# Optimization experiments

Measured on AMD Instinct MI355X. Metric: run time of the kernel, lower is better.

## Reference

```python
import jax, jax.numpy as jnp
import numpy as np
from jax import lax

N = 100000
E = 1600000
IN_C = 128
HID = 128
OUT_C = 64
NUM_CLASSES = 40
BN_EPS = 1e-5


def gcn_conv(x, row, col, W, b):
    # x: [N, F_in] -> [N, F_out]; PyG GCNConv: self-loops + sym normalization
    h = x @ W                                   # [N, F_out]
    loops = jnp.arange(N, dtype=row.dtype)
    r = jnp.concatenate([row, loops])           # [E+N]
    c = jnp.concatenate([col, loops])
    ones = jnp.ones(r.shape[0], dtype=x.dtype)
    deg = jax.ops.segment_sum(ones, c, num_segments=N)
    dinv = jnp.where(deg > 0, lax.rsqrt(deg), jnp.zeros_like(deg))
    norm = dinv[r] * dinv[c]                    # [E+N]
    msg = h[r] * norm[:, None]                  # gather + scale  [E+N, F_out]
    out = jax.ops.segment_sum(msg, c, num_segments=N)
    return out + b


def setup_inputs() -> dict:
    key = jax.random.key(0)
    ks = jax.random.split(key, 16)
    def glorot(k, shape):
        lim = float(np.sqrt(6.0 / (shape[0] + shape[1])))
        return jax.random.uniform(k, shape, jnp.float32, -lim, lim)
    x = jax.random.normal(ks[0], (N, IN_C), jnp.float32)
    edge_index = jax.random.randint(ks[1], (2, E), 0, N, jnp.int64)
    return {
        "x": x,
        "edge_index": edge_index,
        "w1": glorot(ks[2], (IN_C, HID)), "b1": jnp.zeros((HID,), jnp.float32),
        "w2": glorot(ks[3], (HID, HID)), "b2": jnp.zeros((HID,), jnp.float32),
        "bn_gamma": jnp.ones((HID,), jnp.float32), "bn_beta": jnp.zeros((HID,), jnp.float32),
        "bn_mean": jnp.zeros((HID,), jnp.float32), "bn_var": jnp.ones((HID,), jnp.float32),
        "cls_w": glorot(ks[4], (HID, OUT_C)), "cls_b": jnp.zeros((OUT_C,), jnp.float32),
        "sim_w": glorot(ks[5], (HID, NUM_CLASSES)), "sim_b": jnp.zeros((NUM_CLASSES,), jnp.float32),
        "hom_w": glorot(ks[6], (HID, 1)), "hom_b": jnp.zeros((1,), jnp.float32),
        "ent_w": glorot(ks[7], (HID, 1)), "ent_b": jnp.zeros((1,), jnp.float32),
    }


def reference(x, edge_index, w1, b1, w2, b2, bn_gamma, bn_beta, bn_mean, bn_var,
              cls_w, cls_b, sim_w, sim_b, hom_w, hom_b, ent_w, ent_b):
    row, col = edge_index[0], edge_index[1]
    # layer 1: GCNConv -> BN (eval) -> ReLU (dropout is identity in eval)
    h = gcn_conv(x, row, col, w1, b1)
    h = (h - bn_mean) * lax.rsqrt(bn_var + BN_EPS) * bn_gamma + bn_beta
    h = jax.nn.relu(h)
    # layer 2
    h = gcn_conv(h, row, col, w2, b2)
    main_out = jax.nn.log_softmax(h @ cls_w + cls_b, axis=1)
    sim_out = jax.nn.softmax(h @ sim_w + sim_b, axis=1)
    hom_out = jax.nn.sigmoid((h @ hom_w + hom_b)[:, 0])
    ent_out = jax.nn.sigmoid((h @ ent_w + ent_b)[:, 0])
    return (main_out, sim_out, hom_out, ent_out)
```

## Files before the change

### kernel.cpp

```cpp
#include <hip/hip_runtime.h>
#include <hip/hip_bf16.h>
#include <math.h>

#define N_NODES 100000
#define N_EDGES 1600000
#define F 128
#define OUT_C 64
#define NUM_CLASSES 40
#define BN_EPS 1e-5f

#define NBUCK 782
#define BCAP 4096
#define FILL_BLOCKS 512
#define EPB ((N_EDGES + FILL_BLOCKS - 1) / FILL_BLOCKS)
#define FILL_ITERS 13

#define PSC 0
#define POF 128
#define PFB2 256

typedef __hip_bfloat16 bf16;
typedef __attribute__((ext_vector_type(8))) short bf16x8;
typedef __attribute__((ext_vector_type(4))) float f32x4;

struct ParamSegs {
    const void* src[16];
    int dst[16];
};

__device__ __forceinline__ float uasf(unsigned u) { return __uint_as_float(u); }
__device__ __forceinline__ unsigned f2bu(float f) {
    bf16 h = __float2bfloat16(f);
    return (unsigned)*(unsigned short*)&h;
}
__device__ __forceinline__ float ldp(const void* p, int i, int isf) {
    return isf ? ((const float*)p)[i] : __bfloat162float(((const bf16*)p)[i]);
}
__device__ __forceinline__ int load_edge(const int* __restrict__ ei, int which, int i, int i64) {
    size_t elem = (size_t)which * N_EDGES + (size_t)i;
    return i64 ? ei[elem * 2] : ei[elem];
}
__device__ __forceinline__ int detect_isf(const void* x, int t, int* sflag) {
    if (t < 64) {
        unsigned w = ((const unsigned*)x)[t];
        unsigned e = (w >> 23) & 0xFFu;
        unsigned long long m = __ballot(w == 0u || (e >= 90u && e <= 160u));
        if (t == 0) *sflag = (__popcll(m) >= 48) ? 1 : 0;
    }
    __syncthreads();
    return *sflag;
}
__device__ __forceinline__ int detect_i64(const void* ei, int t, int* sflag) {
    if (t < 64) {
        unsigned long long m = __ballot(((const unsigned*)ei)[2 * t + 1] == 0u);
        if (t == 0) *sflag = (__popcll(m) >= 60) ? 1 : 0;
    }
    __syncthreads();
    return *sflag;
}
__device__ __forceinline__ void head_src(const ParamSegs& segs, int c, const void** hp, int* hb,
                                         int* hs) {
    if (c < OUT_C) {
        *hp = segs.src[8];
        *hb = c;
        *hs = OUT_C;
    } else if (c < OUT_C + NUM_CLASSES) {
        *hp = segs.src[10];
        *hb = c - OUT_C;
        *hs = NUM_CLASSES;
    } else if (c == 104) {
        *hp = segs.src[12];
        *hb = 0;
        *hs = 1;
    } else if (c == 105) {
        *hp = segs.src[14];
        *hb = 0;
        *hs = 1;
    } else {
        *hp = nullptr;
        *hb = 0;
        *hs = 0;
    }
}

#define ACC8(u)                                \
    do {                                       \
        a[0] += uasf((u).x << 16);             \
        a[1] += uasf((u).x & 0xFFFF0000u);     \
        a[2] += uasf((u).y << 16);             \
        a[3] += uasf((u).y & 0xFFFF0000u);     \
        a[4] += uasf((u).z << 16);             \
        a[5] += uasf((u).z & 0xFFFF0000u);     \
        a[6] += uasf((u).w << 16);             \
        a[7] += uasf((u).w & 0xFFFF0000u);     \
    } while (0)

__global__ __launch_bounds__(256) void fill2_kernel(const int* __restrict__ ei,
                                                    int* __restrict__ bcur,
                                                    int* __restrict__ srcBuck) {
    __shared__ int hist[NBUCK];
    __shared__ int gbase[NBUCK];
    __shared__ int lcur[NBUCK];
    __shared__ int sflag;
    int blk = blockIdx.x;
    int t = threadIdx.x;
    int i64 = detect_i64(ei, t, &sflag);
    int e0 = blk * EPB;
    int ecnt = N_EDGES - e0;
    if (ecnt > EPB) ecnt = EPB;
    for (int i = t; i < NBUCK; i += 256) hist[i] = 0;
    __syncthreads();
    int ccache[FILL_ITERS];
#pragma unroll
    for (int it = 0; it < FILL_ITERS; ++it) {
        int i = t + it * 256;
        int c = -1;
        if (i < ecnt) {
            c = load_edge(ei, 1, e0 + i, i64);
            atomicAdd(&hist[c >> 7], 1);
        }
        ccache[it] = c;
    }
    __syncthreads();
    for (int i = t; i < NBUCK; i += 256) {
        int c = hist[i];
        gbase[i] = (c > 0) ? atomicAdd(&bcur[i], c) : 0;
        lcur[i] = 0;
    }
    __syncthreads();
#pragma unroll
    for (int it = 0; it < FILL_ITERS; ++it) {
        int i = t + it * 256;
        if (i < ecnt) {
            int c = ccache[it];
            int r = load_edge(ei, 0, e0 + i, i64);
            int b = c >> 7;
            int p = gbase[b] + atomicAdd(&lcur[b], 1);
            if (p < BCAP) srcBuck[b * BCAP + p] = ((c & 127) << 17) | r;
        }
    }
}

__global__ __launch_bounds__(512) void presort_kernel(int* __restrict__ srcBuck,
                                                      const int* __restrict__ bcur,
                                                      int* __restrict__ doffG,
                                                      int* __restrict__ dcntG,
                                                      float* __restrict__ dinv) {
    __shared__ int raw[BCAP];
    __shared__ int sorted[BCAP];
    __shared__ int dcnt[128], doff[128], dcur[128];
    int b = blockIdx.x;
    int t = threadIdx.x;
    int cnt = bcur[b];
    if (cnt > BCAP) cnt = BCAP;
    if (t < 128) dcnt[t] = 0;
    __syncthreads();
    for (int i = t; i < cnt; i += 512) {
        int e = srcBuck[b * BCAP + i];
        raw[i] = e;
        atomicAdd(&dcnt[e >> 17], 1);
    }
    __syncthreads();
    if (t < 128) doff[t] = dcnt[t];
    __syncthreads();
    for (int d = 1; d < 128; d <<= 1) {
        int add = 0;
        if (t < 128 && t >= d) add = doff[t - d];
        __syncthreads();
        if (t < 128) doff[t] += add;
        __syncthreads();
    }
    if (t < 128) {
        doff[t] -= dcnt[t];
        dcur[t] = 0;
    }
    __syncthreads();
    for (int i = t; i < cnt; i += 512) {
        int e = raw[i];
        int d = e >> 17;
        int r = atomicAdd(&dcur[d], 1);
        sorted[doff[d] + r] = e & 0x1FFFF;
    }
    __syncthreads();
    for (int i = t; i < cnt; i += 512) srcBuck[b * BCAP + i] = sorted[i];
    if (t < 128) {
        doffG[(b << 7) + t] = doff[t];
        dcntG[(b << 7) + t] = dcnt[t];
        int n = (b << 7) + t;
        if (n < N_NODES) dinv[n] = rsqrtf((float)(dcnt[t] + 1));
    }
}

#define WPREP_BLOCKS 129
#define CVT_BLOCKS 6250
__global__ __launch_bounds__(256) void cvtxprep_kernel(const void* __restrict__ x,
                                                       ParamSegs segs,
                                                       const float* __restrict__ dinv,
                                                       unsigned short* __restrict__ B16,
                                                       float* __restrict__ params,
                                                       unsigned short* __restrict__ wt) {
    __shared__ int sflag;
    int t = threadIdx.x;
    int bid = blockIdx.x;
    int isf = detect_isf(x, t, &sflag);

    if (bid < 128) {
        int idx = bid * 256 + t;
        if (idx < 16384) {
            int kf = idx >> 7, c = idx & 127;
            const void* hp;
            int hb, hs;
            head_src(segs, c, &hp, &hb, &hs);
            float s = 0.f;
            if (hp) {
                const void* w2 = segs.src[2];
#pragma unroll 8
                for (int j = 0; j < 128; j++) s += ldp(w2, kf * 128 + j, isf) * ldp(hp, j * hs + hb, isf);
            }
            int p = (kf & 15) * 8 + (kf >> 4);
            wt[16384 + c * 128 + p] = (unsigned short)f2bu(s);
        } else {
            int l = idx - 16384;
            int n = l >> 7, k = l & 127;
            wt[n * 128 + k] = (unsigned short)f2bu(ldp(segs.src[0], k * 128 + n, isf));
        }
    } else if (bid == 128) {
        if (t < 128) {
            float s = rsqrtf(ldp(segs.src[7], t, isf) + BN_EPS) * ldp(segs.src[4], t, isf);
            params[PSC + t] = s;
            params[POF + t] =
                ldp(segs.src[1], t, isf) * s + ldp(segs.src[5], t, isf) - ldp(segs.src[6], t, isf) * s;
            const void* hp;
            int hb, hs;
            head_src(segs, t, &hp, &hb, &hs);
            float b = 0.f;
            if (hp) {
                const void* b2 = segs.src[3];
#pragma unroll 8
                for (int j = 0; j < 128; j++) b += ldp(b2, j, isf) * ldp(hp, j * hs + hb, isf);
            }
            if (t < OUT_C) b += ldp(segs.src[9], t, isf);
            else if (t < OUT_C + NUM_CLASSES) b += ldp(segs.src[11], t - OUT_C, isf);
            else if (t == 104) b += ldp(segs.src[13], 0, isf);
            else if (t == 105) b += ldp(segs.src[15], 0, isf);
            params[PFB2 + t] = b;
        }
    } else {
        int i8 = (bid - WPREP_BLOCKS) * 256 + t;
        int n = i8 >> 4;
        float d = dinv[n];
        float v[8];
        if (isf) {
            float4 va = ((const float4*)x)[2 * i8];
            float4 vb = ((const float4*)x)[2 * i8 + 1];
            v[0] = va.x; v[1] = va.y; v[2] = va.z; v[3] = va.w;
            v[4] = vb.x; v[5] = vb.y; v[6] = vb.z; v[7] = vb.w;
        } else {
            uint4 u = ((const uint4*)x)[i8];
            v[0] = uasf(u.x << 16);
            v[1] = uasf(u.x & 0xFFFF0000u);
            v[2] = uasf(u.y << 16);
            v[3] = uasf(u.y & 0xFFFF0000u);
            v[4] = uasf(u.z << 16);
            v[5] = uasf(u.z & 0xFFFF0000u);
            v[6] = uasf(u.w << 16);
            v[7] = uasf(u.w & 0xFFFF0000u);
        }
        uint4 o;
        o.x = f2bu(v[0] * d) | (f2bu(v[1] * d) << 16);
        o.y = f2bu(v[2] * d) | (f2bu(v[3] * d) << 16);
        o.z = f2bu(v[4] * d) | (f2bu(v[5] * d) << 16);
        o.w = f2bu(v[6] * d) | (f2bu(v[7] * d) << 16);
        ((uint4*)B16)[i8] = o;
    }
}

__global__ __launch_bounds__(512) void aggh_kernel(const unsigned short* __restrict__ IN16,
                                                   unsigned short* __restrict__ OUT16,
                                                   const int* __restrict__ srcBuck,
                                                   const int* __restrict__ doffG,
                                                   const int* __restrict__ dcntG,
                                                   const float* __restrict__ dinv,
                                                   int* __restrict__ wcnt) {
    __shared__ int sIdx[BCAP];
    __shared__ int sdoff[128], sdcnt[128];
    __shared__ int sCtl[2];
    int t = threadIdx.x;
    if (t == 0) {
        unsigned xcc;
        asm volatile("s_getreg_b32 %0, hwreg(HW_REG_XCC_ID)" : "=s"(xcc));
        int half = (xcc >> 2) & 1;
        int idx = atomicAdd(&wcnt[half], 1);
        if (idx >= NBUCK) {
            half ^= 1;
            idx = atomicAdd(&wcnt[half], 1);
        }
        sCtl[0] = idx;
        sCtl[1] = half;
    }
    __syncthreads();
    int b = sCtl[0], h = sCtl[1];
    if (b >= NBUCK) return;
    if (t < 128) {
        sdoff[t] = doffG[(b << 7) + t];
        sdcnt[t] = dcntG[(b << 7) + t];
    }
    __syncthreads();
    int cnt = sdoff[127] + sdcnt[127];
    for (int i = t; i < cnt; i += 512) sIdx[i] = srcBuck[b * BCAP + i];
    __syncthreads();

    int g8 = t >> 3;
    int hoff = h * 64 + ((t & 7) << 3);
    int base = b << 7;
    for (int d = g8; d < 128; d += 64) {
        int n = base + d;
        if (n >= N_NODES) break;
        float a[8] = {0.f, 0.f, 0.f, 0.f, 0.f, 0.f, 0.f, 0.f};
        {
            uint4 u = *(const uint4*)(IN16 + ((size_t)n << 7) + hoff);
            ACC8(u);
        }
        int o = sdoff[d], k = sdcnt[d];
        int j = 0;
        for (; j + 8 <= k; j += 8) {
            int s0 = sIdx[o + j + 0], s1 = sIdx[o + j + 1];
            int s2 = sIdx[o + j + 2], s3 = sIdx[o + j + 3];
            int s4 = sIdx[o + j + 4], s5 = sIdx[o + j + 5];
            int s6 = sIdx[o + j + 6], s7 = sIdx[o + j + 7];
            uint4 u0 = *(const uint4*)(IN16 + ((size_t)s0 << 7) + hoff);
            uint4 u1 = *(const uint4*)(IN16 + ((size_t)s1 << 7) + hoff);
            uint4 u2 = *(const uint4*)(IN16 + ((size_t)s2 << 7) + hoff);
            uint4 u3 = *(const uint4*)(IN16 + ((size_t)s3 << 7) + hoff);
            uint4 u4 = *(const uint4*)(IN16 + ((size_t)s4 << 7) + hoff);
            uint4 u5 = *(const uint4*)(IN16 + ((size_t)s5 << 7) + hoff);
            uint4 u6 = *(const uint4*)(IN16 + ((size_t)s6 << 7) + hoff);
            uint4 u7 = *(const uint4*)(IN16 + ((size_t)s7 << 7) + hoff);
            ACC8(u0);
            ACC8(u1);
            ACC8(u2);
            ACC8(u3);
            ACC8(u4);
            ACC8(u5);
            ACC8(u6);
            ACC8(u7);
        }
        for (; j + 4 <= k; j += 4) {
            int s0 = sIdx[o + j + 0], s1 = sIdx[o + j + 1];
            int s2 = sIdx[o + j + 2], s3 = sIdx[o + j + 3];
            uint4 u0 = *(const uint4*)(IN16 + ((size_t)s0 << 7) + hoff);
            uint4 u1 = *(const uint4*)(IN16 + ((size_t)s1 << 7) + hoff);
            uint4 u2 = *(const uint4*)(IN16 + ((size_t)s2 << 7) + hoff);
            uint4 u3 = *(const uint4*)(IN16 + ((size_t)s3 << 7) + hoff);
            ACC8(u0);
            ACC8(u1);
            ACC8(u2);
            ACC8(u3);
        }
        for (; j < k; j++) {
            int s0 = sIdx[o + j];
            uint4 u0 = *(const uint4*)(IN16 + ((size_t)s0 << 7) + hoff);
            ACC8(u0);
        }
        float dn = dinv[n];
        uint4 pk;
        pk.x = f2bu(a[0] * dn) | (f2bu(a[1] * dn) << 16);
        pk.y = f2bu(a[2] * dn) | (f2bu(a[3] * dn) << 16);
        pk.z = f2bu(a[4] * dn) | (f2bu(a[5] * dn) << 16);
        pk.w = f2bu(a[6] * dn) | (f2bu(a[7] * dn) << 16);
        *(uint4*)(OUT16 + ((size_t)n << 7) + hoff) = pk;
    }
}

__global__ __launch_bounds__(256) void gemm_mfma_kernel(
    const unsigned short* __restrict__ A16, const unsigned short* __restrict__ Wt,
    unsigned short* __restrict__ outB, void* __restrict__ out,
    const float* __restrict__ params, const float* __restrict__ dinv, int mode,
    const void* __restrict__ x) {
    __shared__ float sF1[128], sF2[128];
    __shared__ int sflag;
    int t = threadIdx.x;
    int isf = detect_isf(x, t, &sflag);
    if (t < 128) {
        if (mode) {
            sF1[t] = params[PSC + t];
            sF2[t] = params[POF + t];
        } else {
            sF1[t] = params[PFB2 + t];
        }
    }
    __syncthreads();
    int wave = t >> 6, lane = t & 63, m16 = lane & 15, quad = lane >> 4;
    int rowbase = blockIdx.x * 64 + wave * 16;
    int rA = rowbase + m16;
    if (rA >= N_NODES) rA = N_NODES - 1;
    const size_t abase = (size_t)rA * 128 + (quad << 3);

    f32x4 acc[8];
#pragma unroll
    for (int ct = 0; ct < 8; ct++) acc[ct] = (f32x4){0.f, 0.f, 0.f, 0.f};
#pragma unroll
    for (int kk = 0; kk < 4; kk++) {
        bf16x8 af = *(const bf16x8*)(A16 + abase + kk * 32);
#pragma unroll
        for (int ct = 0; ct < 8; ct++) {
            bf16x8 bfr = *(const bf16x8*)(Wt + (size_t)((ct * 16 + m16) * 128) + kk * 32 + (quad << 3));
            acc[ct] = __builtin_amdgcn_mfma_f32_16x16x32_bf16(af, bfr, acc[ct], 0, 0, 0);
        }
    }

    int r0 = rowbase + quad * 4;
    if (mode) {
        float sc[8], of[8];
#pragma unroll
        for (int ct = 0; ct < 8; ct++) {
            sc[ct] = sF1[ct * 16 + m16];
            of[ct] = sF2[ct * 16 + m16];
        }
#pragma unroll
        for (int reg = 0; reg < 4; reg++) {
            int gr = r0 + reg;
            if (gr >= N_NODES) continue;
            float dn = dinv[gr];
            unsigned pk[4];
#pragma unroll
            for (int i = 0; i < 4; i++) {
                float v0 = fmaxf(acc[2 * i][reg] * sc[2 * i] + of[2 * i], 0.f) * dn;
                float v1 = fmaxf(acc[2 * i + 1][reg] * sc[2 * i + 1] + of[2 * i + 1], 0.f) * dn;
                pk[i] = f2bu(v0) | (f2bu(v1) << 16);
            }
            *(uint4*)(outB + (size_t)gr * 128 + (m16 << 3)) = make_uint4(pk[0], pk[1], pk[2], pk[3]);
        }
    } else {
        const size_t OFF_SIM = (size_t)N_NODES * OUT_C;
        const size_t OFF_HOM = OFF_SIM + (size_t)N_NODES * NUM_CLASSES;
        const size_t OFF_ENT = OFF_HOM + (size_t)N_NODES;
        float* outf = (float*)out;
        bf16* outb = (bf16*)out;
        float fb[8];
#pragma unroll
        for (int ct = 0; ct < 8; ct++) fb[ct] = sF1[ct * 16 + m16];
#define STORE_OUT(idx, v)                        \
    do {                                         \
        if (isf) outf[(idx)] = (v);              \
        else outb[(idx)] = __float2bfloat16(v);  \
    } while (0)
#pragma unroll
        for (int reg = 0; reg < 4; reg++) {
            int gr = r0 + reg;
            bool vrow = (gr < N_NODES);
            float v[8];
#pragma unroll
            for (int ct = 0; ct < 8; ct++) v[ct] = acc[ct][reg] + fb[ct];
            float m = fmaxf(fmaxf(v[0], v[1]), fmaxf(v[2], v[3]));
            m = fmaxf(m, __shfl_xor(m, 1));
            m = fmaxf(m, __shfl_xor(m, 2));
            m = fmaxf(m, __shfl_xor(m, 4));
            m = fmaxf(m, __shfl_xor(m, 8));
            float S = __expf(v[0] - m) + __expf(v[1] - m) + __expf(v[2] - m) + __expf(v[3] - m);
            S += __shfl_xor(S, 1);
            S += __shfl_xor(S, 2);
            S += __shfl_xor(S, 4);
            S += __shfl_xor(S, 8);
            float lS = m + __logf(S);
            if (vrow) {
#pragma unroll
                for (int ct = 0; ct < 4; ct++)
                    STORE_OUT((size_t)gr * OUT_C + ct * 16 + m16, v[ct] - lS);
            }
            bool has6 = (m16 < 8);
            float s4 = v[4], s5 = v[5], s6 = has6 ? v[6] : -INFINITY;
            float m2 = fmaxf(fmaxf(s4, s5), s6);
            m2 = fmaxf(m2, __shfl_xor(m2, 1));
            m2 = fmaxf(m2, __shfl_xor(m2, 2));
            m2 = fmaxf(m2, __shfl_xor(m2, 4));
            m2 = fmaxf(m2, __shfl_xor(m2, 8));
            float e4 = __expf(s4 - m2), e5 = __expf(s5 - m2), e6 = has6 ? __expf(s6 - m2) : 0.f;
            float S2 = e4 + e5 + e6;
            S2 += __shfl_xor(S2, 1);
            S2 += __shfl_xor(S2, 2);
            S2 += __shfl_xor(S2, 4);
            S2 += __shfl_xor(S2, 8);
            float rS2 = 1.f / S2;
            if (vrow) {
                STORE_OUT(OFF_SIM + (size_t)gr * NUM_CLASSES + m16, e4 * rS2);
                STORE_OUT(OFF_SIM + (size_t)gr * NUM_CLASSES + 16 + m16, e5 * rS2);
                if (has6) STORE_OUT(OFF_SIM + (size_t)gr * NUM_CLASSES + 32 + m16, e6 * rS2);
                if (m16 == 8) STORE_OUT(OFF_HOM + gr, 1.f / (1.f + __expf(-v[6])));
                if (m16 == 9) STORE_OUT(OFF_ENT + gr, 1.f / (1.f + __expf(-v[6])));
            }
        }
#undef STORE_OUT
    }
}

extern "C" void kernel_launch(void* const* d_in, const int* in_sizes, int n_in,
                              void* d_out, int out_size, void* d_ws, size_t ws_size,
                              hipStream_t stream) {
    const void* x = d_in[0];
    const int* ei = (const int*)d_in[1];

    char* ws = (char*)d_ws;
    size_t o = 0;
    auto alloc = [&](size_t bytes) {
        size_t r = o;
        o = (o + bytes + 255) & ~(size_t)255;
        return r;
    };
    char* RA = ws + alloc((size_t)51 * 1024 * 1024);
    char* RB = ws + alloc((size_t)26 * 1024 * 1024);
    float* params = (float*)(ws + alloc(2048));
    unsigned short* wt = (unsigned short*)(ws + alloc(65536));
    float* dinv = (float*)(ws + alloc((size_t)N_NODES * 4));
    int* doffG = (int*)(ws + alloc((size_t)NBUCK * 128 * 4));
    int* dcntG = (int*)(ws + alloc((size_t)NBUCK * 128 * 4));
    int* bcur = (int*)(ws + alloc((size_t)(NBUCK + 8) * 4));
    int* wcnt = (int*)(ws + alloc(256));

    int* srcBuck = (int*)RA;
    unsigned short* B16 = (unsigned short*)(RA + 13u * 1024 * 1024);
    unsigned short* G16 = (unsigned short*)RB;

    hipMemsetAsync(bcur, 0, (size_t)((char*)wcnt + 256 - (char*)bcur), stream);

    ParamSegs segs;
    const int srcIdx[16] = {2, 3, 4, 5, 6, 7, 8, 9, 10, 11, 12, 13, 14, 15, 16, 17};
    for (int k = 0; k < 16; k++) {
        segs.src[k] = d_in[srcIdx[k]];
        segs.dst[k] = 0;
    }

    fill2_kernel<<<FILL_BLOCKS, 256, 0, stream>>>(ei, bcur, srcBuck);
    presort_kernel<<<NBUCK, 512, 0, stream>>>(srcBuck, bcur, doffG, dcntG, dinv);
    cvtxprep_kernel<<<WPREP_BLOCKS + CVT_BLOCKS, 256, 0, stream>>>(x, segs, dinv, B16, params, wt);

    const int gemmGrid = (N_NODES + 63) / 64;
    aggh_kernel<<<2 * NBUCK, 512, 0, stream>>>(B16, G16, srcBuck, doffG, dcntG, dinv, wcnt);
    gemm_mfma_kernel<<<gemmGrid, 256, 0, stream>>>(G16, wt, B16, nullptr, params, dinv, 1, x);
    aggh_kernel<<<2 * NBUCK, 512, 0, stream>>>(B16, G16, srcBuck, doffG, dcntG, dinv, wcnt + 2);
    gemm_mfma_kernel<<<gemmGrid, 256, 0, stream>>>(G16, wt + 16384, nullptr, d_out, params, dinv, 0, x);
}
```

Before: 379.4 us.

## Merge fill and x-conversion into one prep kernel, apply source dinv in aggregation

The edge bucketing fill, weight/param prep and x-to-bf16 conversion now run as one launch, so the x conversion no longer waits on presort's dinv. Instead of pre-scaling x rows by dinv during conversion, the first aggregation reads dinv per source edge and applies it with FMAs. The bf16 path reads x directly and skips the conversion. This removes one launch and a serial dependency, but adds a random dinv gather per edge in the first aggregation.

New measurement: 374.7 us. No clear change (-1.2%).

```diff
diff --git a/kernel.cpp b/kernel.cpp
--- a/kernel.cpp
+++ b/kernel.cpp
@@ -11,9 +11,13 @@
 
 #define NBUCK 782
 #define BCAP 4096
-#define FILL_BLOCKS 512
-#define EPB ((N_EDGES + FILL_BLOCKS - 1) / FILL_BLOCKS)
+
+#define PREP_FILL 512
+#define EPB ((N_EDGES + PREP_FILL - 1) / PREP_FILL)
 #define FILL_ITERS 13
+#define PREP_CONST (PREP_FILL + 128)
+#define PREP_CVT (PREP_FILL + 129)
+#define CVT_BLOCKS 6250
 
 #define PSC 0
 #define POF 128
@@ -94,50 +98,124 @@
         a[6] += uasf((u).w << 16);             \
         a[7] += uasf((u).w & 0xFFFF0000u);     \
     } while (0)
-
-__global__ __launch_bounds__(256) void fill2_kernel(const int* __restrict__ ei,
-                                                    int* __restrict__ bcur,
-                                                    int* __restrict__ srcBuck) {
-    __shared__ int hist[NBUCK];
-    __shared__ int gbase[NBUCK];
-    __shared__ int lcur[NBUCK];
+#define ACC8W(u, s_)                                        \
+    do {                                                    \
+        a[0] = fmaf(uasf((u).x << 16), (s_), a[0]);         \
+        a[1] = fmaf(uasf((u).x & 0xFFFF0000u), (s_), a[1]); \
+        a[2] = fmaf(uasf((u).y << 16), (s_), a[2]);         \
+        a[3] = fmaf(uasf((u).y & 0xFFFF0000u), (s_), a[3]); \
+        a[4] = fmaf(uasf((u).z << 16), (s_), a[4]);         \
+        a[5] = fmaf(uasf((u).z & 0xFFFF0000u), (s_), a[5]); \
+        a[6] = fmaf(uasf((u).w << 16), (s_), a[6]);         \
+        a[7] = fmaf(uasf((u).w & 0xFFFF0000u), (s_), a[7]); \
+    } while (0)
+
+__global__ __launch_bounds__(256) void prep_kernel(const void* __restrict__ x,
+                                                   const int* __restrict__ ei, ParamSegs segs,
+                                                   int* __restrict__ bcur,
+                                                   int* __restrict__ srcBuck,
+                                                   float* __restrict__ params,
+                                                   unsigned short* __restrict__ wt,
+                                                   unsigned short* __restrict__ B16) {
     __shared__ int sflag;
-    int blk = blockIdx.x;
     int t = threadIdx.x;
-    int i64 = detect_i64(ei, t, &sflag);
-    int e0 = blk * EPB;
-    int ecnt = N_EDGES - e0;
-    if (ecnt > EPB) ecnt = EPB;
-    for (int i = t; i < NBUCK; i += 256) hist[i] = 0;
-    __syncthreads();
-    int ccache[FILL_ITERS];
-#pragma unroll
-    for (int it = 0; it < FILL_ITERS; ++it) {
-        int i = t + it * 256;
-        int c = -1;
-        if (i < ecnt) {
-            c = load_edge(ei, 1, e0 + i, i64);
-            atomicAdd(&hist[c >> 7], 1);
-        }
-        ccache[it] = c;
-    }
-    __syncthreads();
-    for (int i = t; i < NBUCK; i += 256) {
-        int c = hist[i];
-        gbase[i] = (c > 0) ? atomicAdd(&bcur[i], c) : 0;
-        lcur[i] = 0;
-    }
-    __syncthreads();
-#pragma unroll
-    for (int it = 0; it < FILL_ITERS; ++it) {
-        int i = t + it * 256;
-        if (i < ecnt) {
-            int c = ccache[it];
-            int r = load_edge(ei, 0, e0 + i, i64);
-            int b = c >> 7;
-            int p = gbase[b] + atomicAdd(&lcur[b], 1);
-            if (p < BCAP) srcBuck[b * BCAP + p] = ((c & 127) << 17) | r;
-        }
+    int bid = blockIdx.x;
+
+    if (bid < PREP_FILL) {
+        __shared__ int hist[NBUCK];
+        __shared__ int gbase[NBUCK];
+        __shared__ int lcur[NBUCK];
+        int i64 = detect_i64(ei, t, &sflag);
+        int e0 = bid * EPB;
+        int ecnt = N_EDGES - e0;
+        if (ecnt > EPB) ecnt = EPB;
+        for (int i = t; i < NBUCK; i += 256) hist[i] = 0;
+        __syncthreads();
+        int ccache[FILL_ITERS];
+#pragma unroll
+        for (int it = 0; it < FILL_ITERS; ++it) {
+            int i = t + it * 256;
+            int c = -1;
+            if (i < ecnt) {
+                c = load_edge(ei, 1, e0 + i, i64);
+                atomicAdd(&hist[c >> 7], 1);
+            }
+            ccache[it] = c;
+        }
+        __syncthreads();
+        for (int i = t; i < NBUCK; i += 256) {
+            int c = hist[i];
+            gbase[i] = (c > 0) ? atomicAdd(&bcur[i], c) : 0;
+            lcur[i] = 0;
+        }
+        __syncthreads();
+#pragma unroll
+        for (int it = 0; it < FILL_ITERS; ++it) {
+            int i = t + it * 256;
+            if (i < ecnt) {
+                int c = ccache[it];
+                int r = load_edge(ei, 0, e0 + i, i64);
+                int b = c >> 7;
+                int p = gbase[b] + atomicAdd(&lcur[b], 1);
+                if (p < BCAP) srcBuck[b * BCAP + p] = ((c & 127) << 17) | r;
+            }
+        }
+    } else if (bid < PREP_CONST) {
+        int isf = detect_isf(x, t, &sflag);
+        int idx = (bid - PREP_FILL) * 256 + t;
+        if (idx < 16384) {
+            int kf = idx >> 7, c = idx & 127;
+            const void* hp;
+            int hb, hs;
+            head_src(segs, c, &hp, &hb, &hs);
+            float s = 0.f;
+            if (hp) {
+                const void* w2 = segs.src[2];
+#pragma unroll 8
+                for (int j = 0; j < 128; j++)
+                    s += ldp(w2, kf * 128 + j, isf) * ldp(hp, j * hs + hb, isf);
+            }
+            int p = (kf & 15) * 8 + (kf >> 4);
+            wt[16384 + c * 128 + p] = (unsigned short)f2bu(s);
+        } else {
+            int l = idx - 16384;
+            int n = l >> 7, k = l & 127;
+            wt[n * 128 + k] = (unsigned short)f2bu(ldp(segs.src[0], k * 128 + n, isf));
+        }
+    } else if (bid == PREP_CONST) {
+        int isf = detect_isf(x, t, &sflag);
+        if (t < 128) {
+            float s = rsqrtf(ldp(segs.src[7], t, isf) + BN_EPS) * ldp(segs.src[4], t, isf);
+            params[PSC + t] = s;
+            params[POF + t] = ldp(segs.src[1], t, isf) * s + ldp(segs.src[5], t, isf) -
+                              ldp(segs.src[6], t, isf) * s;
+            const void* hp;
+            int hb, hs;
+            head_src(segs, t, &hp, &hb, &hs);
+            float b = 0.f;
+            if (hp) {
+                const void* b2 = segs.src[3];
+#pragma unroll 8
+                for (int j = 0; j < 128; j++) b += ldp(b2, j, isf) * ldp(hp, j * hs + hb, isf);
+            }
+            if (t < OUT_C) b += ldp(segs.src[9], t, isf);
+            else if (t < OUT_C + NUM_CLASSES) b += ldp(segs.src[11], t - OUT_C, isf);
+            else if (t == 104) b += ldp(segs.src[13], 0, isf);
+            else if (t == 105) b += ldp(segs.src[15], 0, isf);
+            params[PFB2 + t] = b;
+        }
+    } else {
+        int isf = detect_isf(x, t, &sflag);
+        if (!isf) return;
+        int i8 = (bid - PREP_CVT) * 256 + t;
+        float4 va = ((const float4*)x)[2 * i8];
+        float4 vb = ((const float4*)x)[2 * i8 + 1];
+        uint4 o;
+        o.x = f2bu(va.x) | (f2bu(va.y) << 16);
+        o.y = f2bu(va.z) | (f2bu(va.w) << 16);
+        o.z = f2bu(vb.x) | (f2bu(vb.y) << 16);
+        o.w = f2bu(vb.z) | (f2bu(vb.w) << 16);
+        ((uint4*)B16)[i8] = o;
     }
 }
 
@@ -191,91 +269,9 @@
     }
 }
 
-#define WPREP_BLOCKS 129
-#define CVT_BLOCKS 6250
-__global__ __launch_bounds__(256) void cvtxprep_kernel(const void* __restrict__ x,
-                                                       ParamSegs segs,
-                                                       const float* __restrict__ dinv,
-                                                       unsigned short* __restrict__ B16,
-                                                       float* __restrict__ params,
-                                                       unsigned short* __restrict__ wt) {
-    __shared__ int sflag;
-    int t = threadIdx.x;
-    int bid = blockIdx.x;
-    int isf = detect_isf(x, t, &sflag);
-
-    if (bid < 128) {
-        int idx = bid * 256 + t;
-        if (idx < 16384) {
-            int kf = idx >> 7, c = idx & 127;
-            const void* hp;
-            int hb, hs;
-            head_src(segs, c, &hp, &hb, &hs);
-            float s = 0.f;
-            if (hp) {
-                const void* w2 = segs.src[2];
-#pragma unroll 8
-                for (int j = 0; j < 128; j++) s += ldp(w2, kf * 128 + j, isf) * ldp(hp, j * hs + hb, isf);
-            }
-            int p = (kf & 15) * 8 + (kf >> 4);
-            wt[16384 + c * 128 + p] = (unsigned short)f2bu(s);
-        } else {
-            int l = idx - 16384;
-            int n = l >> 7, k = l & 127;
-            wt[n * 128 + k] = (unsigned short)f2bu(ldp(segs.src[0], k * 128 + n, isf));
-        }
-    } else if (bid == 128) {
-        if (t < 128) {
-            float s = rsqrtf(ldp(segs.src[7], t, isf) + BN_EPS) * ldp(segs.src[4], t, isf);
-            params[PSC + t] = s;
-            params[POF + t] =
-                ldp(segs.src[1], t, isf) * s + ldp(segs.src[5], t, isf) - ldp(segs.src[6], t, isf) * s;
-            const void* hp;
-            int hb, hs;
-            head_src(segs, t, &hp, &hb, &hs);
-            float b = 0.f;
-            if (hp) {
-                const void* b2 = segs.src[3];
-#pragma unroll 8
-                for (int j = 0; j < 128; j++) b += ldp(b2, j, isf) * ldp(hp, j * hs + hb, isf);
-            }
-            if (t < OUT_C) b += ldp(segs.src[9], t, isf);
-            else if (t < OUT_C + NUM_CLASSES) b += ldp(segs.src[11], t - OUT_C, isf);
-            else if (t == 104) b += ldp(segs.src[13], 0, isf);
-            else if (t == 105) b += ldp(segs.src[15], 0, isf);
-            params[PFB2 + t] = b;
-        }
-    } else {
-        int i8 = (bid - WPREP_BLOCKS) * 256 + t;
-        int n = i8 >> 4;
-        float d = dinv[n];
-        float v[8];
-        if (isf) {
-            float4 va = ((const float4*)x)[2 * i8];
-            float4 vb = ((const float4*)x)[2 * i8 + 1];
-            v[0] = va.x; v[1] = va.y; v[2] = va.z; v[3] = va.w;
-            v[4] = vb.x; v[5] = vb.y; v[6] = vb.z; v[7] = vb.w;
-        } else {
-            uint4 u = ((const uint4*)x)[i8];
-            v[0] = uasf(u.x << 16);
-            v[1] = uasf(u.x & 0xFFFF0000u);
-            v[2] = uasf(u.y << 16);
-            v[3] = uasf(u.y & 0xFFFF0000u);
-            v[4] = uasf(u.z << 16);
-            v[5] = uasf(u.z & 0xFFFF0000u);
-            v[6] = uasf(u.w << 16);
-            v[7] = uasf(u.w & 0xFFFF0000u);
-        }
-        uint4 o;
-        o.x = f2bu(v[0] * d) | (f2bu(v[1] * d) << 16);
-        o.y = f2bu(v[2] * d) | (f2bu(v[3] * d) << 16);
-        o.z = f2bu(v[4] * d) | (f2bu(v[5] * d) << 16);
-        o.w = f2bu(v[6] * d) | (f2bu(v[7] * d) << 16);
-        ((uint4*)B16)[i8] = o;
-    }
-}
-
-__global__ __launch_bounds__(512) void aggh_kernel(const unsigned short* __restrict__ IN16,
+template <bool SRC1>
+__global__ __launch_bounds__(512) void aggh_kernel(const void* __restrict__ x,
+                                                   const unsigned short* __restrict__ B16,
                                                    unsigned short* __restrict__ OUT16,
                                                    const int* __restrict__ srcBuck,
                                                    const int* __restrict__ doffG,
@@ -285,7 +281,13 @@
     __shared__ int sIdx[BCAP];
     __shared__ int sdoff[128], sdcnt[128];
     __shared__ int sCtl[2];
+    __shared__ int sflag;
     int t = threadIdx.x;
+    const unsigned short* IN = B16;
+    if (SRC1) {
+        int isf = detect_isf(x, t, &sflag);
+        if (!isf) IN = (const unsigned short*)x;
+    }
     if (t == 0) {
         unsigned xcc;
         asm volatile("s_getreg_b32 %0, hwreg(HW_REG_XCC_ID)" : "=s"(xcc));
@@ -316,10 +318,12 @@
     for (int d = g8; d < 128; d += 64) {
         int n = base + d;
         if (n >= N_NODES) break;
+        float dn = dinv[n];
         float a[8] = {0.f, 0.f, 0.f, 0.f, 0.f, 0.f, 0.f, 0.f};
         {
-            uint4 u = *(const uint4*)(IN16 + ((size_t)n << 7) + hoff);
-            ACC8(u);
+            uint4 u = *(const uint4*)(IN + ((size_t)n << 7) + hoff);
+            if (SRC1) ACC8W(u, dn);
+            else ACC8(u);
         }
         int o = sdoff[d], k = sdcnt[d];
         int j = 0;
@@ -328,41 +332,66 @@
             int s2 = sIdx[o + j + 2], s3 = sIdx[o + j + 3];
             int s4 = sIdx[o + j + 4], s5 = sIdx[o + j + 5];
             int s6 = sIdx[o + j + 6], s7 = sIdx[o + j + 7];
-            uint4 u0 = *(const uint4*)(IN16 + ((size_t)s0 << 7) + hoff);
-            uint4 u1 = *(const uint4*)(IN16 + ((size_t)s1 << 7) + hoff);
-            uint4 u2 = *(const uint4*)(IN16 + ((size_t)s2 << 7) + hoff);
-            uint4 u3 = *(const uint4*)(IN16 + ((size_t)s3 << 7) + hoff);
-            uint4 u4 = *(const uint4*)(IN16 + ((size_t)s4 << 7) + hoff);
-            uint4 u5 = *(const uint4*)(IN16 + ((size_t)s5 << 7) + hoff);
-            uint4 u6 = *(const uint4*)(IN16 + ((size_t)s6 << 7) + hoff);
-            uint4 u7 = *(const uint4*)(IN16 + ((size_t)s7 << 7) + hoff);
-            ACC8(u0);
-            ACC8(u1);
-            ACC8(u2);
-            ACC8(u3);
-            ACC8(u4);
-            ACC8(u5);
-            ACC8(u6);
-            ACC8(u7);
+            uint4 u0 = *(const uint4*)(IN + ((size_t)s0 << 7) + hoff);
+            uint4 u1 = *(const uint4*)(IN + ((size_t)s1 << 7) + hoff);
+            uint4 u2 = *(const uint4*)(IN + ((size_t)s2 << 7) + hoff);
+            uint4 u3 = *(const uint4*)(IN + ((size_t)s3 << 7) + hoff);
+            uint4 u4 = *(const uint4*)(IN + ((size_t)s4 << 7) + hoff);
+            uint4 u5 = *(const uint4*)(IN + ((size_t)s5 << 7) + hoff);
+            uint4 u6 = *(const uint4*)(IN + ((size_t)s6 << 7) + hoff);
+            uint4 u7 = *(const uint4*)(IN + ((size_t)s7 << 7) + hoff);
+            if (SRC1) {
+                float f0 = dinv[s0], f1 = dinv[s1], f2 = dinv[s2], f3 = dinv[s3];
+                float f4 = dinv[s4], f5 = dinv[s5], f6 = dinv[s6], f7 = dinv[s7];
+                ACC8W(u0, f0);
+                ACC8W(u1, f1);
+                ACC8W(u2, f2);
+                ACC8W(u3, f3);
+                ACC8W(u4, f4);
+                ACC8W(u5, f5);
+                ACC8W(u6, f6);
+                ACC8W(u7, f7);
+            } else {
+                ACC8(u0);
+                ACC8(u1);
+                ACC8(u2);
+                ACC8(u3);
+                ACC8(u4);
+                ACC8(u5);
+                ACC8(u6);
+                ACC8(u7);
+            }
         }
         for (; j + 4 <= k; j += 4) {
             int s0 = sIdx[o + j + 0], s1 = sIdx[o + j + 1];
             int s2 = sIdx[o + j + 2], s3 = sIdx[o + j + 3];
-            uint4 u0 = *(const uint4*)(IN16 + ((size_t)s0 << 7) + hoff);
-            uint4 u1 = *(const uint4*)(IN16 + ((size_t)s1 << 7) + hoff);
-            uint4 u2 = *(const uint4*)(IN16 + ((size_t)s2 << 7) + hoff);
-            uint4 u3 = *(const uint4*)(IN16 + ((size_t)s3 << 7) + hoff);
-            ACC8(u0);
-            ACC8(u1);
-            ACC8(u2);
-            ACC8(u3);
+            uint4 u0 = *(const uint4*)(IN + ((size_t)s0 << 7) + hoff);
+            uint4 u1 = *(const uint4*)(IN + ((size_t)s1 << 7) + hoff);
+            uint4 u2 = *(const uint4*)(IN + ((size_t)s2 << 7) + hoff);
+            uint4 u3 = *(const uint4*)(IN + ((size_t)s3 << 7) + hoff);
+            if (SRC1) {
+                float f0 = dinv[s0], f1 = dinv[s1], f2 = dinv[s2], f3 = dinv[s3];
+                ACC8W(u0, f0);
+                ACC8W(u1, f1);
+                ACC8W(u2, f2);
+                ACC8W(u3, f3);
+            } else {
+                ACC8(u0);
+                ACC8(u1);
+                ACC8(u2);
+                ACC8(u3);
+            }
         }
         for (; j < k; j++) {
             int s0 = sIdx[o + j];
-            uint4 u0 = *(const uint4*)(IN16 + ((size_t)s0 << 7) + hoff);
-            ACC8(u0);
-        }
-        float dn = dinv[n];
+            uint4 u0 = *(const uint4*)(IN + ((size_t)s0 << 7) + hoff);
+            if (SRC1) {
+                float f0 = dinv[s0];
+                ACC8W(u0, f0);
+            } else {
+                ACC8(u0);
+            }
+        }
         uint4 pk;
         pk.x = f2bu(a[0] * dn) | (f2bu(a[1] * dn) << 16);
         pk.y = f2bu(a[2] * dn) | (f2bu(a[3] * dn) << 16);
@@ -530,13 +559,16 @@
         segs.dst[k] = 0;
     }
 
-    fill2_kernel<<<FILL_BLOCKS, 256, 0, stream>>>(ei, bcur, srcBuck);
+    prep_kernel<<<PREP_CVT + CVT_BLOCKS, 256, 0, stream>>>(x, ei, segs, bcur, srcBuck, params,
+                                                           wt, B16);
     presort_kernel<<<NBUCK, 512, 0, stream>>>(srcBuck, bcur, doffG, dcntG, dinv);
-    cvtxprep_kernel<<<WPREP_BLOCKS + CVT_BLOCKS, 256, 0, stream>>>(x, segs, dinv, B16, params, wt);
 
     const int gemmGrid = (N_NODES + 63) / 64;
-    aggh_kernel<<<2 * NBUCK, 512, 0, stream>>>(B16, G16, srcBuck, doffG, dcntG, dinv, wcnt);
+    aggh_kernel<true><<<2 * NBUCK, 512, 0, stream>>>(x, B16, G16, srcBuck, doffG, dcntG, dinv,
+                                                     wcnt);
     gemm_mfma_kernel<<<gemmGrid, 256, 0, stream>>>(G16, wt, B16, nullptr, params, dinv, 1, x);
-    aggh_kernel<<<2 * NBUCK, 512, 0, stream>>>(B16, G16, srcBuck, doffG, dcntG, dinv, wcnt + 2);
-    gemm_mfma_kernel<<<gemmGrid, 256, 0, stream>>>(G16, wt + 16384, nullptr, d_out, params, dinv, 0, x);
-}
+    aggh_kernel<false><<<2 * NBUCK, 512, 0, stream>>>(x, B16, G16, srcBuck, doffG, dcntG, dinv,
+                                                      wcnt + 2);
+    gemm_mfma_kernel<<<gemmGrid, 256, 0, stream>>>(G16, wt + 16384, nullptr, d_out, params, dinv,
+                                                   0, x);
+}
```
